# Performance work log

Measured on AMD Instinct MI355X. Metric: run time of the kernel, lower is better.

Reference implementation:

```python
import jax, jax.numpy as jnp
import numpy as np

B, DZ, DS, DH = 8192, 1024, 64, 4096

def setup_inputs() -> dict:
    key = jax.random.key(0)
    ks = jax.random.split(key, 8)
    r1 = 1.0 / np.sqrt(DZ)   # W1 init range (last dim dz)
    r2 = 1.0 / np.sqrt(DH)   # W2 init range (last dim dim_hidden)
    rc = 1.0 / np.sqrt(DS)   # C init range
    return {
        "z": jax.random.normal(ks[0], (B, DZ), jnp.float32),
        "s": jax.random.normal(ks[1], (B, DS), jnp.float32),
        "A": jnp.full((DZ,), 0.95, jnp.float32),
        "W1": jax.random.uniform(ks[2], (DH, DZ), jnp.float32, -r1, r1),
        "W2": jax.random.uniform(ks[3], (DZ, DH), jnp.float32, -r2, r2),
        "h1": jax.random.normal(ks[4], (DH,), jnp.float32),
        "h2": jax.random.normal(ks[5], (DZ,), jnp.float32),
        "C": jax.random.uniform(ks[6], (DZ, DS), jnp.float32, -rc, rc),
    }

def reference(z, s, A, W1, W2, h1, h2, C):
    # PLRNN step, W_trial=False, mean_center=False, noise=0:
    # z' = A*z + relu(z @ W1.T + h1) @ W2.T + h2 + s @ C.T
    z_activated = jax.nn.relu(z @ W1.T + h1)          # [B, DH]
    return A * z + z_activated @ W2.T + h2 + s @ C.T  # [B, DZ]
```

## Files before the change

### kernel.cpp

```cpp
#include <hip/hip_runtime.h>

#define BB 8192
#define DZ 1024
#define DS 64
#define DH 4096
#define KEXT (DH + DS)

typedef float floatx4 __attribute__((ext_vector_type(4)));
typedef __bf16 bf16x8 __attribute__((ext_vector_type(8)));
typedef __bf16 bf16x4 __attribute__((ext_vector_type(4)));
typedef __attribute__((address_space(1))) void* as1_void_ptr;
typedef __attribute__((address_space(3))) void* as3_void_ptr;

#define WAIT_VM0   3952
#define WAIT_VM6   3958
#define WAIT_LGKM0 49279

__device__ __forceinline__ void async_copy16(const void* g, void* l) {
    __builtin_amdgcn_global_load_lds((as1_void_ptr)g, (as3_void_ptr)l, 16, 0, 0);
}

__device__ __forceinline__ bf16x4 cvt4(float4 v) {
    bf16x4 o = { (__bf16)v.x, (__bf16)v.y, (__bf16)v.z, (__bf16)v.w };
    return o;
}

__global__ void prep_all(const float* __restrict__ z, const float* __restrict__ W1,
                         const float* __restrict__ W2, const float* __restrict__ C,
                         const float* __restrict__ s,
                         __bf16* __restrict__ zb, __bf16* __restrict__ W1b,
                         __bf16* __restrict__ B2b, __bf16* __restrict__ Hb) {
    const int b = blockIdx.x, t = threadIdx.x;
    if (b < 8192) {
        int i = b * 256 + t;
        *(bf16x4*)(zb + (size_t)i * 4) = cvt4(((const float4*)z)[i]);
    } else if (b < 12288) {
        int i = (b - 8192) * 256 + t;
        *(bf16x4*)(W1b + (size_t)i * 4) = cvt4(((const float4*)W1)[i]);
    } else if (b < 13312) {
        int j = b - 12288;
        const float* wrow = W2 + (size_t)j * DH;
        const float* crow = C + (size_t)j * DS;
        __bf16* orow = B2b + (size_t)j * KEXT;
        for (int c = t; c < 520; c += 256) {
            int h = c * 8;
            const float* src = (h < DH) ? (wrow + h) : (crow + (h - DH));
            *(bf16x4*)(orow + h)     = cvt4(*(const float4*)(src));
            *(bf16x4*)(orow + h + 4) = cvt4(*(const float4*)(src + 4));
        }
    } else {
        int i = (b - 13312) * 256 + t;
        int r = i >> 4, k = (i & 15) * 4;
        float4 v = *(const float4*)(s + (size_t)r * DS + k);
        *(bf16x4*)(Hb + (size_t)r * KEXT + DH + k) = cvt4(v);
    }
}


__global__ __launch_bounds__(512, 4) void gemm1_relu(
    const __bf16* __restrict__ Ag, const __bf16* __restrict__ Bg,
    const float* __restrict__ h1, __bf16* __restrict__ Hb)
{
    constexpr int ldA = DZ, ldB = DZ, KITER = DZ / 64;
    __shared__ __align__(16) __bf16 As[256 * 64];
    __shared__ __align__(16) __bf16 Bs[128 * 64];

    const int tid = threadIdx.x;
    const int wave = tid >> 6, lane = tid & 63;
    const int wm = wave >> 1, wn = wave & 1;
    const int row0 = blockIdx.x * 256;
    const int col0 = blockIdx.y * 128;

    const __bf16* pA = Ag + (size_t)(row0 + (tid >> 2)) * ldA + (tid & 3) * 8;
    const __bf16* pB = Bg + (size_t)(col0 + ((tid >> 2) & 127)) * ldB + (tid & 3) * 8;
    __bf16* lA = As + wave * 512;
    __bf16* lB = Bs + wave * 512;

    const __bf16* Afrag = As + (wm * 64 + (lane & 15)) * 32 + (lane >> 4) * 8;
    const __bf16* Bfrag = Bs + (wn * 64 + (lane & 15)) * 32 + (lane >> 4) * 8;

    floatx4 acc[4][4];
#pragma unroll
    for (int i = 0; i < 4; ++i)
#pragma unroll
        for (int j = 0; j < 4; ++j) acc[i][j] = (floatx4)0.0f;

    for (int kt = 0; kt < KITER; ++kt) {
        const __bf16* ak = pA + kt * 64;
        const __bf16* bk = pB + kt * 64;
        async_copy16(ak,                           lA);
        async_copy16(ak + (size_t)128 * ldA,       lA + 4096);
        async_copy16(ak + 32,                      lA + 8192);
        async_copy16(ak + (size_t)128 * ldA + 32,  lA + 8192 + 4096);
        async_copy16(bk,                           lB);
        async_copy16(bk + 32,                      lB + 4096);
        __builtin_amdgcn_s_waitcnt(0);
        __syncthreads();

#pragma unroll
        for (int ks = 0; ks < 2; ++ks) {
            bf16x8 af[4], bfr[4];
#pragma unroll
            for (int i = 0; i < 4; ++i) af[i] = *(const bf16x8*)(Afrag + ks * 8192 + i * 16 * 32);
#pragma unroll
            for (int j = 0; j < 4; ++j) bfr[j] = *(const bf16x8*)(Bfrag + ks * 4096 + j * 16 * 32);
#pragma unroll
            for (int i = 0; i < 4; ++i)
#pragma unroll
                for (int j = 0; j < 4; ++j)
                    acc[i][j] = __builtin_amdgcn_mfma_f32_16x16x32_bf16(af[i], bfr[j], acc[i][j], 0, 0, 0);
        }
        __syncthreads();
    }

    const int r0 = row0 + wm * 64 + (lane >> 4) * 4;
    const int c0 = col0 + wn * 64 + (lane & 15);
#pragma unroll
    for (int i = 0; i < 4; ++i) {
#pragma unroll
        for (int j = 0; j < 4; ++j) {
            int c = c0 + j * 16;
            float bias = h1[c];
#pragma unroll
            for (int rg = 0; rg < 4; ++rg) {
                int r = r0 + i * 16 + rg;
                float v = acc[i][j][rg] + bias;
                v = v > 0.0f ? v : 0.0f;
                Hb[(size_t)r * KEXT + c] = (__bf16)v;
            }
        }
    }
}

__global__ __launch_bounds__(512, 2) void gemm2_out(
    const __bf16* __restrict__ Ag, const __bf16* __restrict__ Bg,
    const float* __restrict__ Adiag, const float* __restrict__ h2,
    const __bf16* __restrict__ zb, float* __restrict__ out)
{
    constexpr int ldA = KEXT, ldB = KEXT, KITER = KEXT / 64;
    __shared__ __align__(16) __bf16 As[2 * 256 * 64];
    __shared__ __align__(16) __bf16 Bs[2 * 128 * 64];

    const int tid = threadIdx.x;
    const int wave = tid >> 6, lane = tid & 63;
    const int wm = wave >> 1, wn = wave & 1;
    const int row0 = blockIdx.x * 256;
    const int col0 = blockIdx.y * 128;

    const __bf16* pA = Ag + (size_t)(row0 + (tid >> 2)) * ldA + (tid & 3) * 8;
    const __bf16* pB = Bg + (size_t)(col0 + ((tid >> 2) & 127)) * ldB + (tid & 3) * 8;

    const __bf16* Afrag = As + (wm * 64 + (lane & 15)) * 32 + (lane >> 4) * 8;
    const __bf16* Bfrag = Bs + (wn * 64 + (lane & 15)) * 32 + (lane >> 4) * 8;

    floatx4 acc[4][4];
#pragma unroll
    for (int i = 0; i < 4; ++i)
#pragma unroll
        for (int j = 0; j < 4; ++j) acc[i][j] = (floatx4)0.0f;

    auto issue = [&](int kt, int q) {
        const __bf16* ak = pA + kt * 64;
        const __bf16* bk = pB + kt * 64;
        __bf16* lA = As + q * 16384 + wave * 512;
        __bf16* lB = Bs + q * 8192  + wave * 512;
        async_copy16(ak,                           lA);
        async_copy16(ak + (size_t)128 * ldA,       lA + 4096);
        async_copy16(ak + 32,                      lA + 8192);
        async_copy16(ak + (size_t)128 * ldA + 32,  lA + 8192 + 4096);
        async_copy16(bk,                           lB);
        async_copy16(bk + 32,                      lB + 4096);
    };

    issue(0, 0);

    for (int kt = 0; kt < KITER; ++kt) {
        const int p = kt & 1;
        if (kt + 1 < KITER) {
            issue(kt + 1, p ^ 1);
            __builtin_amdgcn_s_waitcnt(WAIT_VM6);
        } else {
            __builtin_amdgcn_s_waitcnt(WAIT_VM0);
        }
        __builtin_amdgcn_s_barrier();

#pragma unroll
        for (int ks = 0; ks < 2; ++ks) {
            const __bf16* Ab = Afrag + p * 16384 + ks * 8192;
            const __bf16* Bb = Bfrag + p * 8192  + ks * 4096;
            bf16x8 af[4], bfr[4];
#pragma unroll
            for (int i = 0; i < 4; ++i) af[i] = *(const bf16x8*)(Ab + i * 16 * 32);
#pragma unroll
            for (int j = 0; j < 4; ++j) bfr[j] = *(const bf16x8*)(Bb + j * 16 * 32);
#pragma unroll
            for (int i = 0; i < 4; ++i)
#pragma unroll
                for (int j = 0; j < 4; ++j)
                    acc[i][j] = __builtin_amdgcn_mfma_f32_16x16x32_bf16(af[i], bfr[j], acc[i][j], 0, 0, 0);
        }

        __builtin_amdgcn_s_waitcnt(WAIT_LGKM0);
        __builtin_amdgcn_s_barrier();
    }

    const int r0 = row0 + wm * 64 + (lane >> 4) * 4;
    const int c0 = col0 + wn * 64 + (lane & 15);
#pragma unroll
    for (int i = 0; i < 4; ++i) {
#pragma unroll
        for (int j = 0; j < 4; ++j) {
            const int c = c0 + j * 16;
            const float aj = Adiag[c];
            const float hj = h2[c];
#pragma unroll
            for (int rg = 0; rg < 4; ++rg) {
                const int r = r0 + i * 16 + rg;
                out[(size_t)r * DZ + c] =
                    acc[i][j][rg] + aj * (float)zb[(size_t)r * DZ + c] + hj;
            }
        }
    }
}


extern "C" void kernel_launch(void* const* d_in, const int* in_sizes, int n_in,
                              void* d_out, int out_size, void* d_ws, size_t ws_size,
                              hipStream_t stream) {
    const float* z  = (const float*)d_in[0];
    const float* s  = (const float*)d_in[1];
    const float* A  = (const float*)d_in[2];
    const float* W1 = (const float*)d_in[3];
    const float* W2 = (const float*)d_in[4];
    const float* h1 = (const float*)d_in[5];
    const float* h2 = (const float*)d_in[6];
    const float* C  = (const float*)d_in[7];
    float* out = (float*)d_out;

    char* ws = (char*)d_ws;
    size_t offHb  = 0;
    size_t offZb  = offHb  + (size_t)BB * KEXT * 2;
    size_t offW1b = offZb  + (size_t)BB * DZ * 2;
    size_t offB2b = offW1b + (size_t)DH * DZ * 2;
    __bf16* Hb  = (__bf16*)(ws + offHb);
    __bf16* zb  = (__bf16*)(ws + offZb);
    __bf16* W1b = (__bf16*)(ws + offW1b);
    __bf16* B2b = (__bf16*)(ws + offB2b);

    prep_all<<<13824, 256, 0, stream>>>(z, W1, W2, C, s, zb, W1b, B2b, Hb);
    gemm1_relu<<<dim3(BB / 256, DH / 128), 512, 0, stream>>>(zb, W1b, h1, Hb);
    gemm2_out<<<dim3(BB / 256, DZ / 128), 512, 0, stream>>>(Hb, B2b, A, h2, zb, out);
}
```

Measured before the change: 259.6 us.

## Load B fragments directly from global and double-buffer A tiles in both GEMMs

Both GEMM kernels shrink to 128x128 tiles with 256 threads. The B operand is now read straight from global memory into registers instead of being staged through LDS, and only the A tile goes through LDS. gemm1 also gains double-buffered async A loads in place of its synchronous single buffer. This cuts LDS traffic and footprint and raises occupancy. In exchange, B is no longer shared through LDS, so each wave re-reads B from global memory and loses reuse across the two row waves.

```diff
diff --git a/kernel.cpp b/kernel.cpp
--- a/kernel.cpp
+++ b/kernel.cpp
@@ -13,7 +13,7 @@
 typedef __attribute__((address_space(3))) void* as3_void_ptr;
 
 #define WAIT_VM0   3952
-#define WAIT_VM6   3958
+#define WAIT_VM4   3956
 #define WAIT_LGKM0 49279
 
 __device__ __forceinline__ void async_copy16(const void* g, void* l) {
@@ -57,27 +57,22 @@
 }
 
 
-__global__ __launch_bounds__(512, 4) void gemm1_relu(
+__global__ __launch_bounds__(256) void gemm1_relu(
     const __bf16* __restrict__ Ag, const __bf16* __restrict__ Bg,
     const float* __restrict__ h1, __bf16* __restrict__ Hb)
 {
     constexpr int ldA = DZ, ldB = DZ, KITER = DZ / 64;
-    __shared__ __align__(16) __bf16 As[256 * 64];
-    __shared__ __align__(16) __bf16 Bs[128 * 64];
+    __shared__ __align__(16) __bf16 As[2 * 128 * 64];
 
     const int tid = threadIdx.x;
     const int wave = tid >> 6, lane = tid & 63;
     const int wm = wave >> 1, wn = wave & 1;
-    const int row0 = blockIdx.x * 256;
+    const int row0 = blockIdx.x * 128;
     const int col0 = blockIdx.y * 128;
 
     const __bf16* pA = Ag + (size_t)(row0 + (tid >> 2)) * ldA + (tid & 3) * 8;
-    const __bf16* pB = Bg + (size_t)(col0 + ((tid >> 2) & 127)) * ldB + (tid & 3) * 8;
-    __bf16* lA = As + wave * 512;
-    __bf16* lB = Bs + wave * 512;
-
+    const __bf16* pBf = Bg + (size_t)(col0 + wn * 64 + (lane & 15)) * ldB + (lane >> 4) * 8;
     const __bf16* Afrag = As + (wm * 64 + (lane & 15)) * 32 + (lane >> 4) * 8;
-    const __bf16* Bfrag = Bs + (wn * 64 + (lane & 15)) * 32 + (lane >> 4) * 8;
 
     floatx4 acc[4][4];
 #pragma unroll
@@ -85,32 +80,52 @@
 #pragma unroll
         for (int j = 0; j < 4; ++j) acc[i][j] = (floatx4)0.0f;
 
+    {
+        __bf16* lA = As + wave * 512;
+        async_copy16(pA,                          lA);
+        async_copy16(pA + (size_t)64 * ldA,       lA + 2048);
+        async_copy16(pA + 32,                     lA + 4096);
+        async_copy16(pA + (size_t)64 * ldA + 32,  lA + 4096 + 2048);
+    }
+
     for (int kt = 0; kt < KITER; ++kt) {
-        const __bf16* ak = pA + kt * 64;
-        const __bf16* bk = pB + kt * 64;
-        async_copy16(ak,                           lA);
-        async_copy16(ak + (size_t)128 * ldA,       lA + 4096);
-        async_copy16(ak + 32,                      lA + 8192);
-        async_copy16(ak + (size_t)128 * ldA + 32,  lA + 8192 + 4096);
-        async_copy16(bk,                           lB);
-        async_copy16(bk + 32,                      lB + 4096);
-        __builtin_amdgcn_s_waitcnt(0);
-        __syncthreads();
+        const int p = kt & 1;
+
+        bf16x8 bfr[2][4];
+#pragma unroll
+        for (int ks = 0; ks < 2; ++ks)
+#pragma unroll
+            for (int j = 0; j < 4; ++j)
+                bfr[ks][j] = *(const bf16x8*)(pBf + (size_t)j * 16 * ldB + kt * 64 + ks * 32);
+
+        if (kt + 1 < KITER) {
+            const __bf16* ak = pA + (kt + 1) * 64;
+            __bf16* lA = As + (p ^ 1) * 8192 + wave * 512;
+            async_copy16(ak,                          lA);
+            async_copy16(ak + (size_t)64 * ldA,       lA + 2048);
+            async_copy16(ak + 32,                     lA + 4096);
+            async_copy16(ak + (size_t)64 * ldA + 32,  lA + 4096 + 2048);
+            __builtin_amdgcn_s_waitcnt(WAIT_VM4);
+        } else {
+            __builtin_amdgcn_s_waitcnt(WAIT_VM0);
+        }
+        __builtin_amdgcn_s_barrier();
 
 #pragma unroll
         for (int ks = 0; ks < 2; ++ks) {
-            bf16x8 af[4], bfr[4];
-#pragma unroll
-            for (int i = 0; i < 4; ++i) af[i] = *(const bf16x8*)(Afrag + ks * 8192 + i * 16 * 32);
-#pragma unroll
-            for (int j = 0; j < 4; ++j) bfr[j] = *(const bf16x8*)(Bfrag + ks * 4096 + j * 16 * 32);
+            bf16x8 af[4];
+#pragma unroll
+            for (int i = 0; i < 4; ++i)
+                af[i] = *(const bf16x8*)(Afrag + p * 8192 + ks * 4096 + i * 16 * 32);
 #pragma unroll
             for (int i = 0; i < 4; ++i)
 #pragma unroll
                 for (int j = 0; j < 4; ++j)
-                    acc[i][j] = __builtin_amdgcn_mfma_f32_16x16x32_bf16(af[i], bfr[j], acc[i][j], 0, 0, 0);
-        }
-        __syncthreads();
+                    acc[i][j] = __builtin_amdgcn_mfma_f32_16x16x32_bf16(af[i], bfr[ks][j], acc[i][j], 0, 0, 0);
+        }
+
+        __builtin_amdgcn_s_waitcnt(WAIT_LGKM0);
+        __builtin_amdgcn_s_barrier();
     }
 
     const int r0 = row0 + wm * 64 + (lane >> 4) * 4;
@@ -132,26 +147,23 @@
     }
 }
 
-__global__ __launch_bounds__(512, 2) void gemm2_out(
+__global__ __launch_bounds__(256) void gemm2_out(
     const __bf16* __restrict__ Ag, const __bf16* __restrict__ Bg,
     const float* __restrict__ Adiag, const float* __restrict__ h2,
     const __bf16* __restrict__ zb, float* __restrict__ out)
 {
     constexpr int ldA = KEXT, ldB = KEXT, KITER = KEXT / 64;
-    __shared__ __align__(16) __bf16 As[2 * 256 * 64];
-    __shared__ __align__(16) __bf16 Bs[2 * 128 * 64];
+    __shared__ __align__(16) __bf16 As[2 * 128 * 64];
 
     const int tid = threadIdx.x;
     const int wave = tid >> 6, lane = tid & 63;
     const int wm = wave >> 1, wn = wave & 1;
-    const int row0 = blockIdx.x * 256;
+    const int row0 = blockIdx.x * 128;
     const int col0 = blockIdx.y * 128;
 
     const __bf16* pA = Ag + (size_t)(row0 + (tid >> 2)) * ldA + (tid & 3) * 8;
-    const __bf16* pB = Bg + (size_t)(col0 + ((tid >> 2) & 127)) * ldB + (tid & 3) * 8;
-
+    const __bf16* pBf = Bg + (size_t)(col0 + wn * 64 + (lane & 15)) * ldB + (lane >> 4) * 8;
     const __bf16* Afrag = As + (wm * 64 + (lane & 15)) * 32 + (lane >> 4) * 8;
-    const __bf16* Bfrag = Bs + (wn * 64 + (lane & 15)) * 32 + (lane >> 4) * 8;
 
     floatx4 acc[4][4];
 #pragma unroll
@@ -159,26 +171,32 @@
 #pragma unroll
         for (int j = 0; j < 4; ++j) acc[i][j] = (floatx4)0.0f;
 
-    auto issue = [&](int kt, int q) {
-        const __bf16* ak = pA + kt * 64;
-        const __bf16* bk = pB + kt * 64;
-        __bf16* lA = As + q * 16384 + wave * 512;
-        __bf16* lB = Bs + q * 8192  + wave * 512;
-        async_copy16(ak,                           lA);
-        async_copy16(ak + (size_t)128 * ldA,       lA + 4096);
-        async_copy16(ak + 32,                      lA + 8192);
-        async_copy16(ak + (size_t)128 * ldA + 32,  lA + 8192 + 4096);
-        async_copy16(bk,                           lB);
-        async_copy16(bk + 32,                      lB + 4096);
-    };
-
-    issue(0, 0);
+    {
+        __bf16* lA = As + wave * 512;
+        async_copy16(pA,                          lA);
+        async_copy16(pA + (size_t)64 * ldA,       lA + 2048);
+        async_copy16(pA + 32,                     lA + 4096);
+        async_copy16(pA + (size_t)64 * ldA + 32,  lA + 4096 + 2048);
+    }
 
     for (int kt = 0; kt < KITER; ++kt) {
         const int p = kt & 1;
+
+        bf16x8 bfr[2][4];
+#pragma unroll
+        for (int ks = 0; ks < 2; ++ks)
+#pragma unroll
+            for (int j = 0; j < 4; ++j)
+                bfr[ks][j] = *(const bf16x8*)(pBf + (size_t)j * 16 * ldB + kt * 64 + ks * 32);
+
         if (kt + 1 < KITER) {
-            issue(kt + 1, p ^ 1);
-            __builtin_amdgcn_s_waitcnt(WAIT_VM6);
+            const __bf16* ak = pA + (kt + 1) * 64;
+            __bf16* lA = As + (p ^ 1) * 8192 + wave * 512;
+            async_copy16(ak,                          lA);
+            async_copy16(ak + (size_t)64 * ldA,       lA + 2048);
+            async_copy16(ak + 32,                     lA + 4096);
+            async_copy16(ak + (size_t)64 * ldA + 32,  lA + 4096 + 2048);
+            __builtin_amdgcn_s_waitcnt(WAIT_VM4);
         } else {
             __builtin_amdgcn_s_waitcnt(WAIT_VM0);
         }
@@ -186,18 +204,15 @@
 
 #pragma unroll
         for (int ks = 0; ks < 2; ++ks) {
-            const __bf16* Ab = Afrag + p * 16384 + ks * 8192;
-            const __bf16* Bb = Bfrag + p * 8192  + ks * 4096;
-            bf16x8 af[4], bfr[4];
-#pragma unroll
-            for (int i = 0; i < 4; ++i) af[i] = *(const bf16x8*)(Ab + i * 16 * 32);
-#pragma unroll
-            for (int j = 0; j < 4; ++j) bfr[j] = *(const bf16x8*)(Bb + j * 16 * 32);
+            bf16x8 af[4];
+#pragma unroll
+            for (int i = 0; i < 4; ++i)
+                af[i] = *(const bf16x8*)(Afrag + p * 8192 + ks * 4096 + i * 16 * 32);
 #pragma unroll
             for (int i = 0; i < 4; ++i)
 #pragma unroll
                 for (int j = 0; j < 4; ++j)
-                    acc[i][j] = __builtin_amdgcn_mfma_f32_16x16x32_bf16(af[i], bfr[j], acc[i][j], 0, 0, 0);
+                    acc[i][j] = __builtin_amdgcn_mfma_f32_16x16x32_bf16(af[i], bfr[ks][j], acc[i][j], 0, 0, 0);
         }
 
         __builtin_amdgcn_s_waitcnt(WAIT_LGKM0);
@@ -248,6 +263,6 @@
     __bf16* B2b = (__bf16*)(ws + offB2b);
 
     prep_all<<<13824, 256, 0, stream>>>(z, W1, W2, C, s, zb, W1b, B2b, Hb);
-    gemm1_relu<<<dim3(BB / 256, DH / 128), 512, 0, stream>>>(zb, W1b, h1, Hb);
-    gemm2_out<<<dim3(BB / 256, DZ / 128), 512, 0, stream>>>(Hb, B2b, A, h2, zb, out);
-}
+    gemm1_relu<<<dim3(BB / 128, DH / 128), 256, 0, stream>>>(zb, W1b, h1, Hb);
+    gemm2_out<<<dim3(BB / 128, DZ / 128), 256, 0, stream>>>(Hb, B2b, A, h2, zb, out);
+}
```

Result: slower. 411.1 us (+58.3%).
